# Performance work log

Measured on AMD Instinct MI355X. Metric: run time of the kernel, lower is better.

The kernel has to match this reference:

```python
import jax, jax.numpy as jnp
import numpy as np

P = 7                 # ROI pool output size (7,7)
SCALE = 1.0 / 16.0    # spatial_scale


def setup_inputs() -> dict:
    key = jax.random.key(0)
    ks = jax.random.split(key, 8)
    C, H, W = 512, 32, 32
    N = 128
    n_classes = 21
    features = jax.random.normal(ks[0], (1, C, H, W), dtype=jnp.float32)
    img_h, img_w = H * 16, W * 16  # image-space size implied by stride 16
    u = jax.random.uniform(ks[1], (N, 4), dtype=jnp.float32)
    x1 = u[:, 0] * (img_w - 32.0)
    y1 = u[:, 1] * (img_h - 32.0)
    x2 = x1 + 16.0 + u[:, 2] * (img_w - 1.0 - 16.0 - x1)
    y2 = y1 + 16.0 + u[:, 3] * (img_h - 1.0 - 16.0 - y1)
    rois = jnp.stack([jnp.zeros(N), x1, y1, x2, y2], axis=1).astype(jnp.float32)
    d_in = C * P * P

    def lin(k, fi, fo):
        return (jax.random.normal(k, (fi, fo), dtype=jnp.float32) / np.float32(np.sqrt(fi)))

    return {
        "features": features,
        "rois": rois,
        "W6": lin(ks[2], d_in, 4096), "b6": jnp.zeros((4096,), jnp.float32),
        "W7": lin(ks[3], 4096, 4096), "b7": jnp.zeros((4096,), jnp.float32),
        "Ws": lin(ks[4], 4096, n_classes), "bs": jnp.zeros((n_classes,), jnp.float32),
        "Wb": lin(ks[5], 4096, n_classes * 4), "bb": jnp.zeros((n_classes * 4,), jnp.float32),
    }


def roi_adaptive_max_pool(features, rois):
    # features: [1, C, H, W]; rois: [N, 5] (col 0 = batch idx, stripped as in torch)
    feats = features[0]                       # [C, H, W]
    C, H, W = feats.shape
    boxes = jnp.floor(rois[:, 1:] * SCALE).astype(jnp.int32)  # .long() trunc, coords >= 0
    x1, y1, x2, y2 = boxes[:, 0], boxes[:, 1], boxes[:, 2], boxes[:, 3]
    h = y2 - y1 + 1  # inclusive slicing roi[1]:roi[3]+1
    w = x2 - x1 + 1
    i = jnp.arange(P)
    # AdaptiveMaxPool2d bin boundaries: start = floor(i*h/P), end = ceil((i+1)*h/P)
    rs = y1[:, None] + (i[None, :] * h[:, None]) // P                       # [N, P]
    re = y1[:, None] + ((i[None, :] + 1) * h[:, None] + (P - 1)) // P
    cs = x1[:, None] + (i[None, :] * w[:, None]) // P
    ce = x1[:, None] + ((i[None, :] + 1) * w[:, None] + (P - 1)) // P
    MBr = -(-H // P)  # max rows per bin
    MBc = -(-W // P)  # max cols per bin
    neg_inf = jnp.float32(-jnp.inf)
    # row stage: max over each bin's rows, all columns kept
    ridx = rs[:, :, None] + jnp.arange(MBr)                                 # [N, P, MBr]
    rmask = ridx < re[:, :, None]
    ridx = jnp.clip(ridx, 0, H - 1)
    rowg = feats[:, ridx, :]                                                # [C, N, P, MBr, W]
    rowg = jnp.where(rmask[None, :, :, :, None], rowg, neg_inf)
    rowmax = rowg.max(axis=3).transpose(1, 0, 2, 3)                         # [N, C, P, W]
    # col stage: max over each bin's columns
    cidx = cs[:, :, None] + jnp.arange(MBc)                                 # [N, P, MBc]
    cmask = cidx < ce[:, :, None]
    cidx = jnp.clip(cidx, 0, W - 1)
    colg = jax.vmap(lambda rm, ci: rm[:, :, ci])(rowmax, cidx)              # [N, C, P, P, MBc]
    colg = jnp.where(cmask[:, None, None, :, :], colg, neg_inf)
    return colg.max(axis=-1)                                                # [N, C, P, P]


def reference(features, rois, W6, b6, W7, b7, Ws, bs, Wb, bb):
    pooled = roi_adaptive_max_pool(features, rois)          # [N, C, 7, 7]
    x = pooled.reshape(pooled.shape[0], -1)                 # [N, C*49]
    x = jax.nn.relu(x @ W6 + b6)                            # fc6 (dropout off: eval)
    x = jax.nn.relu(x @ W7 + b7)                            # fc7
    cls_prob = jax.nn.softmax(x @ Ws + bs, axis=1)          # [N, n_classes]
    bbox_pred = x @ Wb + bb                                 # [N, n_classes*4]
    return jnp.concatenate([cls_prob, bbox_pred], axis=1)   # [N, n_classes*5]
```

## Files before the change

### kernel.cpp

```cpp
#include <hip/hip_runtime.h>
#include <stdint.h>
#include <math.h>


typedef short short8 __attribute__((ext_vector_type(8)));
typedef float f32x4 __attribute__((ext_vector_type(4)));

__device__ __forceinline__ uint32_t pack_hilo(float x) {
  uint32_t xb = __float_as_uint(x);
  uint32_t hi = (xb + 0x7fffu + ((xb >> 16) & 1u)) >> 16;
  float hf = __uint_as_float(hi << 16);
  float d = x - hf;
  uint32_t db = __float_as_uint(d);
  uint32_t lo = (db + 0x7fffu + ((db >> 16) & 1u)) >> 16;
  return (lo << 16) | (hi & 0xffffu);
}

__device__ __forceinline__ short8 mk8(uint32_t a, uint32_t b, uint32_t c, uint32_t d) {
  union { uint32_t u[4]; short8 s; } x;
  x.u[0] = a; x.u[1] = b; x.u[2] = c; x.u[3] = d;
  return x.s;
}

__global__ void transpose_k(const float* __restrict__ in, float* __restrict__ out) {
  __shared__ float sm[64][65];
  int bc = blockIdx.x & 7;
  int bp = blockIdx.x >> 3;
  int c0 = bc * 64, p0 = bp * 64;
  int tx = threadIdx.x & 63, ty = threadIdx.x >> 6;
  for (int r = ty; r < 64; r += 4)
    sm[r][tx] = in[(size_t)(c0 + r) * 1024 + p0 + tx];
  __syncthreads();
  for (int r = ty; r < 64; r += 4)
    out[(size_t)(p0 + r) * 512 + c0 + tx] = sm[tx][r];
}

__global__ void pool_k(const float* __restrict__ feats_t, const float* __restrict__ rois,
                       uint32_t* __restrict__ Apk) {
  int n = blockIdx.x >> 1, half = blockIdx.x & 1;
  int t = threadIdx.x;
  int c = half * 256 + t;
  __shared__ uint32_t sm[256 * 49];

  float r1 = rois[n * 5 + 1], r2 = rois[n * 5 + 2];
  float r3 = rois[n * 5 + 3], r4 = rois[n * 5 + 4];
  int x1 = (int)floorf(r1 * 0.0625f);
  int y1 = (int)floorf(r2 * 0.0625f);
  int x2 = (int)floorf(r3 * 0.0625f);
  int y2 = (int)floorf(r4 * 0.0625f);
  int h = y2 - y1 + 1, w = x2 - x1 + 1;

  for (int cell = 0; cell < 49; ++cell) {
    int i = cell / 7, j = cell % 7;
    int rs = y1 + (i * h) / 7;
    int re = y1 + ((i + 1) * h + 6) / 7;  re = min(re, rs + 5);
    int cs = x1 + (j * w) / 7;
    int ce = x1 + ((j + 1) * w + 6) / 7;  ce = min(ce, cs + 5);
    float m = -INFINITY;
    for (int r = rs; r < re; ++r)
      for (int cc = cs; cc < ce; ++cc)
        m = fmaxf(m, feats_t[(size_t)(r * 32 + cc) * 512 + c]);
    sm[t * 49 + cell] = pack_hilo(m);
  }
  __syncthreads();
  uint32_t* dst = Apk + (size_t)n * 25088 + (size_t)half * 12544;
  for (int i = t; i < 256 * 49; i += 256) dst[i] = sm[i];
}

__global__ __launch_bounds__(256, 2)
void gemm_splitk(const uint32_t* __restrict__ Apk, const float* __restrict__ W,
                 float* __restrict__ partials, int Ktot, int ksteps, int ksh) {
  const int t = threadIdx.x;
  const int wvid = t >> 6, lane = t & 63;
  const int bid = blockIdx.x;
  const int nb = bid >> ksh;
  const int ks = bid & ((1 << ksh) - 1);
  const int n0 = nb << 7;
  const int kbase = ks * (ksteps << 5);

  __shared__ uint32_t lsA[128 * 36];
  __shared__ uint32_t lsB[128 * 36];

  const int nloc = t & 127, khalf = t >> 7;
  const float* wg = W + (size_t)(kbase + khalf * 16) * 4096 + n0 + nloc;

  const int arow_in = (lane >> 3);
  const int achk = lane & 7;
  const uint32_t* ag = Apk + (size_t)(wvid * 32 + arow_in) * Ktot + kbase + achk * 4;

  f32x4 acc[2][8];
#pragma unroll
  for (int i = 0; i < 2; i++)
#pragma unroll
    for (int j = 0; j < 8; j++) acc[i][j] = f32x4{0.f, 0.f, 0.f, 0.f};

  float wc0[16], wc1[16];
  uint4 ac0[4], ac1[4];

#pragma unroll
  for (int i = 0; i < 16; i++) wc0[i] = __builtin_nontemporal_load(wg + (size_t)i * 4096);
#pragma unroll
  for (int j = 0; j < 4; j++) ac0[j] = *(const uint4*)(ag + (size_t)j * 8 * Ktot);

  const int lr = lane & 15, kk = lane >> 4;

  auto step = [&](int s, float (&wc)[16], float (&wn)[16], uint4 (&ac)[4], uint4 (&an)[4]) {
    uint32_t pk[16];
#pragma unroll
    for (int i = 0; i < 16; i++) pk[i] = pack_hilo(wc[i]);

    __syncthreads();
#pragma unroll
    for (int i = 0; i < 4; i++)
      *(uint4*)&lsB[nloc * 36 + khalf * 16 + i * 4] =
          make_uint4(pk[i * 4], pk[i * 4 + 1], pk[i * 4 + 2], pk[i * 4 + 3]);
#pragma unroll
    for (int j = 0; j < 4; j++)
      *(uint4*)&lsA[(wvid * 32 + j * 8 + arow_in) * 36 + achk * 4] = ac[j];
    __syncthreads();

    if (s + 1 < ksteps) {
      const float* wgs = wg + (size_t)(s + 1) * 32 * 4096;
#pragma unroll
      for (int i = 0; i < 16; i++) wn[i] = __builtin_nontemporal_load(wgs + (size_t)i * 4096);
      const uint32_t* ags = ag + (size_t)(s + 1) * 32;
#pragma unroll
      for (int j = 0; j < 4; j++) an[j] = *(const uint4*)(ags + (size_t)j * 8 * Ktot);
    }

    short8 ahi[2], alo[2];
#pragma unroll
    for (int fm = 0; fm < 2; fm++) {
      int rb = (wvid * 32 + fm * 16 + lr) * 36 + kk * 8;
      uint4 q0 = *(const uint4*)&lsA[rb];
      uint4 q1 = *(const uint4*)&lsA[rb + 4];
      ahi[fm] = mk8(__builtin_amdgcn_perm(q0.y, q0.x, 0x05040100u),
                    __builtin_amdgcn_perm(q0.w, q0.z, 0x05040100u),
                    __builtin_amdgcn_perm(q1.y, q1.x, 0x05040100u),
                    __builtin_amdgcn_perm(q1.w, q1.z, 0x05040100u));
      alo[fm] = mk8(__builtin_amdgcn_perm(q0.y, q0.x, 0x07060302u),
                    __builtin_amdgcn_perm(q0.w, q0.z, 0x07060302u),
                    __builtin_amdgcn_perm(q1.y, q1.x, 0x07060302u),
                    __builtin_amdgcn_perm(q1.w, q1.z, 0x07060302u));
    }
#pragma unroll
    for (int fn = 0; fn < 8; fn++) {
      int rb = (fn * 16 + lr) * 36 + kk * 8;
      uint4 q0 = *(const uint4*)&lsB[rb];
      uint4 q1 = *(const uint4*)&lsB[rb + 4];
      short8 bhi = mk8(__builtin_amdgcn_perm(q0.y, q0.x, 0x05040100u),
                       __builtin_amdgcn_perm(q0.w, q0.z, 0x05040100u),
                       __builtin_amdgcn_perm(q1.y, q1.x, 0x05040100u),
                       __builtin_amdgcn_perm(q1.w, q1.z, 0x05040100u));
      short8 blo = mk8(__builtin_amdgcn_perm(q0.y, q0.x, 0x07060302u),
                       __builtin_amdgcn_perm(q0.w, q0.z, 0x07060302u),
                       __builtin_amdgcn_perm(q1.y, q1.x, 0x07060302u),
                       __builtin_amdgcn_perm(q1.w, q1.z, 0x07060302u));
#pragma unroll
      for (int fm = 0; fm < 2; fm++) {
        acc[fm][fn] = __builtin_amdgcn_mfma_f32_16x16x32_bf16(ahi[fm], bhi, acc[fm][fn], 0, 0, 0);
        acc[fm][fn] = __builtin_amdgcn_mfma_f32_16x16x32_bf16(ahi[fm], blo, acc[fm][fn], 0, 0, 0);
        acc[fm][fn] = __builtin_amdgcn_mfma_f32_16x16x32_bf16(alo[fm], bhi, acc[fm][fn], 0, 0, 0);
      }
    }
  };

  for (int s = 0; s < ksteps; s += 2) {
    step(s, wc0, wc1, ac0, ac1);
    if (s + 1 < ksteps) step(s + 1, wc1, wc0, ac1, ac0);
  }

  float* pout = partials + (size_t)ks * 524288;
  const int rq = lane >> 4;
#pragma unroll
  for (int fm = 0; fm < 2; fm++)
#pragma unroll
    for (int fn = 0; fn < 8; fn++)
#pragma unroll
      for (int r = 0; r < 4; r++) {
        int row = wvid * 32 + fm * 16 + rq * 4 + r;
        int col = n0 + fn * 16 + lr;
        __builtin_nontemporal_store(acc[fm][fn][r], pout + (size_t)row * 4096 + col);
      }
}

__global__ void reduce_k(const float* __restrict__ partials, const float* __restrict__ bias,
                         uint32_t* __restrict__ pkout, float* __restrict__ fout, int KS) {
  int base = (blockIdx.x * 256 + threadIdx.x) * 4;
  float4 s = make_float4(0.f, 0.f, 0.f, 0.f);
  for (int k = 0; k < KS; k++) {
    const float4 p = *(const float4*)(partials + (size_t)k * 524288 + base);
    s.x += p.x; s.y += p.y; s.z += p.z; s.w += p.w;
  }
  const float4 bv = *(const float4*)(bias + (base & 4095));
  s.x = fmaxf(s.x + bv.x, 0.f); s.y = fmaxf(s.y + bv.y, 0.f);
  s.z = fmaxf(s.z + bv.z, 0.f); s.w = fmaxf(s.w + bv.w, 0.f);
  if (pkout) {
    uint4 o = make_uint4(pack_hilo(s.x), pack_hilo(s.y), pack_hilo(s.z), pack_hilo(s.w));
    *(uint4*)(pkout + base) = o;
  } else {
    *(float4*)(fout + base) = s;
  }
}

__global__ void heads_k(const float* __restrict__ x2, const float* __restrict__ Ws,
                        const float* __restrict__ bs, const float* __restrict__ Wb,
                        const float* __restrict__ bb, float* __restrict__ out) {
  int n = blockIdx.x, t = threadIdx.x;
  int j = t & 127, kq = t >> 7;
  float a0 = 0.f, a1 = 0.f, a2 = 0.f, a3 = 0.f;
  if (j < 105) {
    const float* xp = x2 + (size_t)n * 4096 + kq * 1024;
    const float* wq;
    int stride;
    if (j < 21) { wq = Ws + (size_t)kq * 1024 * 21 + j; stride = 21; }
    else        { wq = Wb + (size_t)kq * 1024 * 84 + (j - 21); stride = 84; }
    for (int k = 0; k < 1024; k += 4) {
      const float4 xv = *(const float4*)(xp + k);
      a0 += xv.x * wq[(size_t)k * stride];
      a1 += xv.y * wq[(size_t)(k + 1) * stride];
      a2 += xv.z * wq[(size_t)(k + 2) * stride];
      a3 += xv.w * wq[(size_t)(k + 3) * stride];
    }
  }
  __shared__ float sacc[512];
  __shared__ float slog[105];
  sacc[t] = (a0 + a1) + (a2 + a3);
  __syncthreads();
  if (t < 105)
    slog[t] = (sacc[t] + sacc[t + 128]) + (sacc[t + 256] + sacc[t + 384]) +
              (t < 21 ? bs[t] : bb[t - 21]);
  __syncthreads();
  if (t < 105) {
    float v = slog[t];
    if (t < 21) {
      float m = slog[0];
      for (int q = 1; q < 21; q++) m = fmaxf(m, slog[q]);
      float ssum = 0.f;
      for (int q = 0; q < 21; q++) ssum += expf(slog[q] - m);
      v = expf(v - m) / ssum;
    }
    out[(size_t)n * 105 + t] = v;
  }
}

extern "C" void kernel_launch(void* const* d_in, const int* in_sizes, int n_in,
                              void* d_out, int out_size, void* d_ws, size_t ws_size,
                              hipStream_t stream) {
  const float* feats = (const float*)d_in[0];
  const float* rois  = (const float*)d_in[1];
  const float* W6 = (const float*)d_in[2];
  const float* b6 = (const float*)d_in[3];
  const float* W7 = (const float*)d_in[4];
  const float* b7 = (const float*)d_in[5];
  const float* Wsp = (const float*)d_in[6];
  const float* bsp = (const float*)d_in[7];
  const float* Wbp = (const float*)d_in[8];
  const float* bbp = (const float*)d_in[9];
  float* out = (float*)d_out;

  char* ws = (char*)d_ws;
  size_t o = 0;
  float*    feats_t = (float*)(ws + o);    o += (size_t)512 * 1024 * 4;
  uint32_t* Apk     = (uint32_t*)(ws + o); o += (size_t)128 * 25088 * 4;
  uint32_t* A2pk    = (uint32_t*)(ws + o); o += (size_t)128 * 4096 * 4;
  float*    x2      = (float*)(ws + o);    o += (size_t)128 * 4096 * 4;
  size_t fixed = o;
  int KS = 16;
  while (KS > 1 && fixed + (size_t)KS * 524288 * 4 > ws_size) KS >>= 1;
  float* partials = (float*)(ws + o);
  int ksh = (KS == 16) ? 4 : (KS == 8) ? 3 : (KS == 4) ? 2 : (KS == 2) ? 1 : 0;
  int ksh7 = (ksh > 3) ? 3 : ksh;
  int KS7 = 1 << ksh7;

  hipLaunchKernelGGL(transpose_k, dim3(128), dim3(256), 0, stream, feats, feats_t);
  hipLaunchKernelGGL(pool_k, dim3(256), dim3(256), 0, stream, feats_t, rois, Apk);
  hipLaunchKernelGGL(gemm_splitk, dim3(32 << ksh), dim3(256), 0, stream,
                     Apk, W6, partials, 25088, 25088 / (KS * 32), ksh);
  hipLaunchKernelGGL(reduce_k, dim3(512), dim3(256), 0, stream,
                     partials, b6, A2pk, (float*)nullptr, KS);
  hipLaunchKernelGGL(gemm_splitk, dim3(32 << ksh7), dim3(256), 0, stream,
                     A2pk, W7, partials, 4096, 4096 / (KS7 * 32), ksh7);
  hipLaunchKernelGGL(reduce_k, dim3(512), dim3(256), 0, stream,
                     partials, b7, (uint32_t*)nullptr, x2, KS7);
  hipLaunchKernelGGL(heads_k, dim3(128), dim3(512), 0, stream,
                     x2, Wsp, bsp, Wbp, bbp, out);
}
```

Before: 935.7 us.

## Store bf16 hi/lo splits in separate planes and restructure GEMM LDS pipeline

Activations and weights are now kept as separate bf16-hi and bf16-lo planes instead of interleaved hi/lo words. The MFMA fragments can then be read straight from LDS without per-fragment perm unpacking. The GEMM main loop is restructured so the next global loads are issued before the MFMA work on the current tile, using four LDS planes with a smaller row stride. This reduces VALU perm work and LDS traffic in the bandwidth-bound FC layers. The cost is more sync points and changed register pressure.

```diff
diff --git a/kernel.cpp b/kernel.cpp
--- a/kernel.cpp
+++ b/kernel.cpp
@@ -16,9 +16,23 @@
   return (lo << 16) | (hi & 0xffffu);
 }
 
-__device__ __forceinline__ short8 mk8(uint32_t a, uint32_t b, uint32_t c, uint32_t d) {
-  union { uint32_t u[4]; short8 s; } x;
-  x.u[0] = a; x.u[1] = b; x.u[2] = c; x.u[3] = d;
+__device__ __forceinline__ void pack_pair(float x0, float x1,
+                                          uint32_t& hw, uint32_t& lw) {
+  uint32_t u0 = __float_as_uint(x0), u1 = __float_as_uint(x1);
+  uint32_t r0 = (u0 + 0x7fffu + ((u0 >> 16) & 1u)) & 0xffff0000u;
+  uint32_t r1 = (u1 + 0x7fffu + ((u1 >> 16) & 1u)) & 0xffff0000u;
+  hw = r1 | (r0 >> 16);
+  float d0 = x0 - __uint_as_float(r0);
+  float d1 = x1 - __uint_as_float(r1);
+  uint32_t v0 = __float_as_uint(d0), v1 = __float_as_uint(d1);
+  uint32_t s0 = (v0 + 0x7fffu + ((v0 >> 16) & 1u)) & 0xffff0000u;
+  uint32_t s1 = (v1 + 0x7fffu + ((v1 >> 16) & 1u)) & 0xffff0000u;
+  lw = s1 | (s0 >> 16);
+}
+
+__device__ __forceinline__ short8 lds_frag(const uint32_t* p) {
+  union { uint4 q; short8 s; } x;
+  x.q = *(const uint4*)p;
   return x.s;
 }
 
@@ -36,7 +50,7 @@
 }
 
 __global__ void pool_k(const float* __restrict__ feats_t, const float* __restrict__ rois,
-                       uint32_t* __restrict__ Apk) {
+                       uint32_t* __restrict__ Ahi, uint32_t* __restrict__ Alo) {
   int n = blockIdx.x >> 1, half = blockIdx.x & 1;
   int t = threadIdx.x;
   int c = half * 256 + t;
@@ -63,30 +77,35 @@
     sm[t * 49 + cell] = pack_hilo(m);
   }
   __syncthreads();
-  uint32_t* dst = Apk + (size_t)n * 25088 + (size_t)half * 12544;
-  for (int i = t; i < 256 * 49; i += 256) dst[i] = sm[i];
+  uint32_t* dh = Ahi + (size_t)n * 12544 + (size_t)half * 6272;
+  uint32_t* dl = Alo + (size_t)n * 12544 + (size_t)half * 6272;
+  for (int i = t; i < 6272; i += 256) {
+    uint32_t w0 = sm[2 * i], w1 = sm[2 * i + 1];
+    dh[i] = __builtin_amdgcn_perm(w1, w0, 0x05040100u);
+    dl[i] = __builtin_amdgcn_perm(w1, w0, 0x07060302u);
+  }
 }
 
 __global__ __launch_bounds__(256, 2)
-void gemm_splitk(const uint32_t* __restrict__ Apk, const float* __restrict__ W,
-                 float* __restrict__ partials, int Ktot, int ksteps, int ksh) {
+void gemm_splitk(const uint32_t* __restrict__ Ahi, const uint32_t* __restrict__ Alo,
+                 const float* __restrict__ W, float* __restrict__ partials,
+                 int Khalf, int ksteps, int ksh) {
   const int t = threadIdx.x;
   const int wvid = t >> 6, lane = t & 63;
-  const int bid = blockIdx.x;
-  const int nb = bid >> ksh;
-  const int ks = bid & ((1 << ksh) - 1);
+  const int nb = blockIdx.x >> ksh;
+  const int ks = blockIdx.x & ((1 << ksh) - 1);
   const int n0 = nb << 7;
-  const int kbase = ks * (ksteps << 5);
-
-  __shared__ uint32_t lsA[128 * 36];
-  __shared__ uint32_t lsB[128 * 36];
+  const int kbase2 = ks * (ksteps << 4);
+
+  __shared__ uint32_t lds[4][128 * 20];
 
   const int nloc = t & 127, khalf = t >> 7;
-  const float* wg = W + (size_t)(kbase + khalf * 16) * 4096 + n0 + nloc;
-
-  const int arow_in = (lane >> 3);
-  const int achk = lane & 7;
-  const uint32_t* ag = Apk + (size_t)(wvid * 32 + arow_in) * Ktot + kbase + achk * 4;
+  const float* wg = W + ((size_t)kbase2 * 2 + khalf * 16) * 4096 + n0 + nloc;
+
+  const int arow = wvid * 32 + (lane >> 1);
+  const int aco = (lane & 1) * 8;
+  const uint32_t* agh = Ahi + (size_t)arow * Khalf + kbase2 + aco;
+  const uint32_t* agl = Alo + (size_t)arow * Khalf + kbase2 + aco;
 
   f32x4 acc[2][8];
 #pragma unroll
@@ -94,80 +113,88 @@
 #pragma unroll
     for (int j = 0; j < 8; j++) acc[i][j] = f32x4{0.f, 0.f, 0.f, 0.f};
 
-  float wc0[16], wc1[16];
-  uint4 ac0[4], ac1[4];
-
-#pragma unroll
-  for (int i = 0; i < 16; i++) wc0[i] = __builtin_nontemporal_load(wg + (size_t)i * 4096);
-#pragma unroll
-  for (int j = 0; j < 4; j++) ac0[j] = *(const uint4*)(ag + (size_t)j * 8 * Ktot);
+  float wcA[16], wcB[16];
+  uint4 aA[4], aB[4];
+
+  auto issue = [&](float (&wc)[16], uint4 (&av)[4], int s) {
+    const float* wp = wg + (size_t)s * 32 * 4096;
+#pragma unroll
+    for (int i = 0; i < 16; i++) wc[i] = __builtin_nontemporal_load(wp + (size_t)i * 4096);
+    const uint32_t* ph = agh + (size_t)s * 16;
+    const uint32_t* pl = agl + (size_t)s * 16;
+    av[0] = *(const uint4*)(ph);
+    av[1] = *(const uint4*)(ph + 4);
+    av[2] = *(const uint4*)(pl);
+    av[3] = *(const uint4*)(pl + 4);
+  };
+
+  auto pack_w = [&](float (&wc)[16], uint32_t (&hw)[8], uint32_t (&lw)[8]) {
+#pragma unroll
+    for (int j = 0; j < 8; j++) pack_pair(wc[2 * j], wc[2 * j + 1], hw[j], lw[j]);
+  };
+  auto store_tile = [&](uint32_t (&hw)[8], uint32_t (&lw)[8], uint4 (&av)[4]) {
+    *(uint4*)&lds[2][nloc * 20 + khalf * 8]     = make_uint4(hw[0], hw[1], hw[2], hw[3]);
+    *(uint4*)&lds[2][nloc * 20 + khalf * 8 + 4] = make_uint4(hw[4], hw[5], hw[6], hw[7]);
+    *(uint4*)&lds[3][nloc * 20 + khalf * 8]     = make_uint4(lw[0], lw[1], lw[2], lw[3]);
+    *(uint4*)&lds[3][nloc * 20 + khalf * 8 + 4] = make_uint4(lw[4], lw[5], lw[6], lw[7]);
+    *(uint4*)&lds[0][arow * 20 + aco]     = av[0];
+    *(uint4*)&lds[0][arow * 20 + aco + 4] = av[1];
+    *(uint4*)&lds[1][arow * 20 + aco]     = av[2];
+    *(uint4*)&lds[1][arow * 20 + aco + 4] = av[3];
+  };
 
   const int lr = lane & 15, kk = lane >> 4;
 
-  auto step = [&](int s, float (&wc)[16], float (&wn)[16], uint4 (&ac)[4], uint4 (&an)[4]) {
-    uint32_t pk[16];
-#pragma unroll
-    for (int i = 0; i < 16; i++) pk[i] = pack_hilo(wc[i]);
-
-    __syncthreads();
-#pragma unroll
-    for (int i = 0; i < 4; i++)
-      *(uint4*)&lsB[nloc * 36 + khalf * 16 + i * 4] =
-          make_uint4(pk[i * 4], pk[i * 4 + 1], pk[i * 4 + 2], pk[i * 4 + 3]);
-#pragma unroll
-    for (int j = 0; j < 4; j++)
-      *(uint4*)&lsA[(wvid * 32 + j * 8 + arow_in) * 36 + achk * 4] = ac[j];
-    __syncthreads();
-
+  auto mfma_tile = [&]() {
+    short8 ahif[2], alof[2];
+#pragma unroll
+    for (int fm = 0; fm < 2; fm++) {
+      int rb = (wvid * 32 + fm * 16 + lr) * 20 + kk * 4;
+      ahif[fm] = lds_frag(&lds[0][rb]);
+      alof[fm] = lds_frag(&lds[1][rb]);
+    }
+#pragma unroll
+    for (int fn = 0; fn < 8; fn++) {
+      int rb = (fn * 16 + lr) * 20 + kk * 4;
+      short8 bhi = lds_frag(&lds[2][rb]);
+      short8 blo = lds_frag(&lds[3][rb]);
+#pragma unroll
+      for (int fm = 0; fm < 2; fm++) {
+        acc[fm][fn] = __builtin_amdgcn_mfma_f32_16x16x32_bf16(ahif[fm], bhi, acc[fm][fn], 0, 0, 0);
+        acc[fm][fn] = __builtin_amdgcn_mfma_f32_16x16x32_bf16(ahif[fm], blo, acc[fm][fn], 0, 0, 0);
+        acc[fm][fn] = __builtin_amdgcn_mfma_f32_16x16x32_bf16(alof[fm], bhi, acc[fm][fn], 0, 0, 0);
+      }
+    }
+  };
+
+  issue(wcA, aA, 0);
+  if (ksteps > 1) issue(wcB, aB, 1);
+  {
+    uint32_t hw[8], lw[8];
+    pack_w(wcA, hw, lw);
+    store_tile(hw, lw, aA);
+  }
+  __syncthreads();
+
+  for (int s = 0; s < ksteps; s += 2) {
+    if (s + 2 < ksteps) issue(wcA, aA, s + 2);
+    mfma_tile();
     if (s + 1 < ksteps) {
-      const float* wgs = wg + (size_t)(s + 1) * 32 * 4096;
-#pragma unroll
-      for (int i = 0; i < 16; i++) wn[i] = __builtin_nontemporal_load(wgs + (size_t)i * 4096);
-      const uint32_t* ags = ag + (size_t)(s + 1) * 32;
-#pragma unroll
-      for (int j = 0; j < 4; j++) an[j] = *(const uint4*)(ags + (size_t)j * 8 * Ktot);
-    }
-
-    short8 ahi[2], alo[2];
-#pragma unroll
-    for (int fm = 0; fm < 2; fm++) {
-      int rb = (wvid * 32 + fm * 16 + lr) * 36 + kk * 8;
-      uint4 q0 = *(const uint4*)&lsA[rb];
-      uint4 q1 = *(const uint4*)&lsA[rb + 4];
-      ahi[fm] = mk8(__builtin_amdgcn_perm(q0.y, q0.x, 0x05040100u),
-                    __builtin_amdgcn_perm(q0.w, q0.z, 0x05040100u),
-                    __builtin_amdgcn_perm(q1.y, q1.x, 0x05040100u),
-                    __builtin_amdgcn_perm(q1.w, q1.z, 0x05040100u));
-      alo[fm] = mk8(__builtin_amdgcn_perm(q0.y, q0.x, 0x07060302u),
-                    __builtin_amdgcn_perm(q0.w, q0.z, 0x07060302u),
-                    __builtin_amdgcn_perm(q1.y, q1.x, 0x07060302u),
-                    __builtin_amdgcn_perm(q1.w, q1.z, 0x07060302u));
-    }
-#pragma unroll
-    for (int fn = 0; fn < 8; fn++) {
-      int rb = (fn * 16 + lr) * 36 + kk * 8;
-      uint4 q0 = *(const uint4*)&lsB[rb];
-      uint4 q1 = *(const uint4*)&lsB[rb + 4];
-      short8 bhi = mk8(__builtin_amdgcn_perm(q0.y, q0.x, 0x05040100u),
-                       __builtin_amdgcn_perm(q0.w, q0.z, 0x05040100u),
-                       __builtin_amdgcn_perm(q1.y, q1.x, 0x05040100u),
-                       __builtin_amdgcn_perm(q1.w, q1.z, 0x05040100u));
-      short8 blo = mk8(__builtin_amdgcn_perm(q0.y, q0.x, 0x07060302u),
-                       __builtin_amdgcn_perm(q0.w, q0.z, 0x07060302u),
-                       __builtin_amdgcn_perm(q1.y, q1.x, 0x07060302u),
-                       __builtin_amdgcn_perm(q1.w, q1.z, 0x07060302u));
-#pragma unroll
-      for (int fm = 0; fm < 2; fm++) {
-        acc[fm][fn] = __builtin_amdgcn_mfma_f32_16x16x32_bf16(ahi[fm], bhi, acc[fm][fn], 0, 0, 0);
-        acc[fm][fn] = __builtin_amdgcn_mfma_f32_16x16x32_bf16(ahi[fm], blo, acc[fm][fn], 0, 0, 0);
-        acc[fm][fn] = __builtin_amdgcn_mfma_f32_16x16x32_bf16(alo[fm], bhi, acc[fm][fn], 0, 0, 0);
+      uint32_t hw[8], lw[8];
+      pack_w(wcB, hw, lw);
+      __syncthreads();
+      store_tile(hw, lw, aB);
+      __syncthreads();
+      if (s + 3 < ksteps) issue(wcB, aB, s + 3);
+      mfma_tile();
+      if (s + 2 < ksteps) {
+        uint32_t hw2[8], lw2[8];
+        pack_w(wcA, hw2, lw2);
+        __syncthreads();
+        store_tile(hw2, lw2, aA);
+        __syncthreads();
       }
     }
-  };
-
-  for (int s = 0; s < ksteps; s += 2) {
-    step(s, wc0, wc1, ac0, ac1);
-    if (s + 1 < ksteps) step(s + 1, wc1, wc0, ac1, ac0);
   }
 
   float* pout = partials + (size_t)ks * 524288;
@@ -185,8 +212,10 @@
 }
 
 __global__ void reduce_k(const float* __restrict__ partials, const float* __restrict__ bias,
-                         uint32_t* __restrict__ pkout, float* __restrict__ fout, int KS) {
-  int base = (blockIdx.x * 256 + threadIdx.x) * 4;
+                         uint32_t* __restrict__ outhi, uint32_t* __restrict__ outlo,
+                         float* __restrict__ fout, int KS) {
+  int idx = blockIdx.x * 256 + threadIdx.x;
+  int base = idx * 4;
   float4 s = make_float4(0.f, 0.f, 0.f, 0.f);
   for (int k = 0; k < KS; k++) {
     const float4 p = *(const float4*)(partials + (size_t)k * 524288 + base);
@@ -195,9 +224,12 @@
   const float4 bv = *(const float4*)(bias + (base & 4095));
   s.x = fmaxf(s.x + bv.x, 0.f); s.y = fmaxf(s.y + bv.y, 0.f);
   s.z = fmaxf(s.z + bv.z, 0.f); s.w = fmaxf(s.w + bv.w, 0.f);
-  if (pkout) {
-    uint4 o = make_uint4(pack_hilo(s.x), pack_hilo(s.y), pack_hilo(s.z), pack_hilo(s.w));
-    *(uint4*)(pkout + base) = o;
+  if (outhi) {
+    uint32_t h0, l0, h1, l1;
+    pack_pair(s.x, s.y, h0, l0);
+    pack_pair(s.z, s.w, h1, l1);
+    *(uint2*)(outhi + idx * 2) = make_uint2(h0, h1);
+    *(uint2*)(outlo + idx * 2) = make_uint2(l0, l1);
   } else {
     *(float4*)(fout + base) = s;
   }
@@ -262,8 +294,10 @@
   char* ws = (char*)d_ws;
   size_t o = 0;
   float*    feats_t = (float*)(ws + o);    o += (size_t)512 * 1024 * 4;
-  uint32_t* Apk     = (uint32_t*)(ws + o); o += (size_t)128 * 25088 * 4;
-  uint32_t* A2pk    = (uint32_t*)(ws + o); o += (size_t)128 * 4096 * 4;
+  uint32_t* Ahi     = (uint32_t*)(ws + o); o += (size_t)128 * 12544 * 4;
+  uint32_t* Alo     = (uint32_t*)(ws + o); o += (size_t)128 * 12544 * 4;
+  uint32_t* A2hi    = (uint32_t*)(ws + o); o += (size_t)128 * 2048 * 4;
+  uint32_t* A2lo    = (uint32_t*)(ws + o); o += (size_t)128 * 2048 * 4;
   float*    x2      = (float*)(ws + o);    o += (size_t)128 * 4096 * 4;
   size_t fixed = o;
   int KS = 16;
@@ -274,15 +308,15 @@
   int KS7 = 1 << ksh7;
 
   hipLaunchKernelGGL(transpose_k, dim3(128), dim3(256), 0, stream, feats, feats_t);
-  hipLaunchKernelGGL(pool_k, dim3(256), dim3(256), 0, stream, feats_t, rois, Apk);
+  hipLaunchKernelGGL(pool_k, dim3(256), dim3(256), 0, stream, feats_t, rois, Ahi, Alo);
   hipLaunchKernelGGL(gemm_splitk, dim3(32 << ksh), dim3(256), 0, stream,
-                     Apk, W6, partials, 25088, 25088 / (KS * 32), ksh);
+                     Ahi, Alo, W6, partials, 12544, 25088 / (KS * 32), ksh);
   hipLaunchKernelGGL(reduce_k, dim3(512), dim3(256), 0, stream,
-                     partials, b6, A2pk, (float*)nullptr, KS);
+                     partials, b6, A2hi, A2lo, (float*)nullptr, KS);
   hipLaunchKernelGGL(gemm_splitk, dim3(32 << ksh7), dim3(256), 0, stream,
-                     A2pk, W7, partials, 4096, 4096 / (KS7 * 32), ksh7);
+                     A2hi, A2lo, W7, partials, 2048, 4096 / (KS7 * 32), ksh7);
   hipLaunchKernelGGL(reduce_k, dim3(512), dim3(256), 0, stream,
-                     partials, b7, (uint32_t*)nullptr, x2, KS7);
+                     partials, b7, (uint32_t*)nullptr, (uint32_t*)nullptr, x2, KS7);
   hipLaunchKernelGGL(heads_k, dim3(128), dim3(512), 0, stream,
                      x2, Wsp, bsp, Wbp, bbp, out);
 }
```

Measured after the change: 932.0 us. About the same (-0.4%).
